# Kernel optimization log

Hardware: AMD Instinct MI355X
Metric: run time of the kernel (lower is better)

The kernel has to match this reference:

```python
import jax, jax.numpy as jnp
import numpy as np

N_NODES = 50000
N_EDGES = 800000
IN_C, HID, OUT_C = 128, 128, 16
N_GRAPHS = 128


def setup_inputs() -> dict:
    key = jax.random.key(0)
    ks = jax.random.split(key, 8)
    x = jax.random.normal(ks[0], (N_NODES, IN_C), dtype=jnp.float32)
    edge_index = jax.random.randint(ks[1], (2, N_EDGES), 0, N_NODES, dtype=jnp.int64)
    batch = jnp.sort(jax.random.randint(ks[2], (N_NODES,), 0, N_GRAPHS, dtype=jnp.int64))
    s1 = 1.0 / np.sqrt(IN_C)
    s2 = 1.0 / np.sqrt(HID)
    W1 = jax.random.normal(ks[3], (IN_C, HID), dtype=jnp.float32) * s1
    b1 = jnp.zeros((HID,), dtype=jnp.float32)
    W2 = jax.random.normal(ks[4], (HID, HID), dtype=jnp.float32) * s2
    b2 = jnp.zeros((HID,), dtype=jnp.float32)
    Wfc = jax.random.normal(ks[5], (HID, OUT_C), dtype=jnp.float32) * s2
    bfc = jnp.zeros((OUT_C,), dtype=jnp.float32)
    return {"x": x, "edge_index": edge_index, "batch": batch,
            "W1": W1, "b1": b1, "W2": W2, "b2": b2, "Wfc": Wfc, "bfc": bfc}


def _gcn_conv(x, W, b, src, dst, deg_inv_sqrt, n_nodes):
    # linear transform first (PyG order), then normalized sparse aggregation
    h = x @ W  # [N, H]
    norm = deg_inv_sqrt[src] * deg_inv_sqrt[dst]  # [E+N] (self-loops appended)
    msgs = h[src] * norm[:, None]  # [E+N, H] dominant gather
    agg = jax.ops.segment_sum(msgs, dst, num_segments=n_nodes)
    return agg + b


def reference(x, edge_index, batch, W1, b1, W2, b2, Wfc, bfc):
    n = x.shape[0]
    loops = jnp.arange(n, dtype=edge_index.dtype)
    src = jnp.concatenate([edge_index[0], loops])
    dst = jnp.concatenate([edge_index[1], loops])
    # symmetric normalization with self-loops: deg computed on dst
    deg = jax.ops.segment_sum(jnp.ones_like(src, dtype=x.dtype), dst, num_segments=n)
    deg_inv_sqrt = jnp.where(deg > 0, jax.lax.rsqrt(jnp.maximum(deg, 1.0)), 0.0)

    h = jax.nn.relu(_gcn_conv(x, W1, b1, src, dst, deg_inv_sqrt, n))
    h = jax.nn.relu(_gcn_conv(h, W2, b2, src, dst, deg_inv_sqrt, n))

    # global mean pool over graph ids
    sums = jax.ops.segment_sum(h, batch, num_segments=N_GRAPHS)
    counts = jax.ops.segment_sum(jnp.ones((n,), dtype=h.dtype), batch, num_segments=N_GRAPHS)
    pooled = sums / jnp.maximum(counts, 1.0)[:, None]  # [G, H]

    logits = pooled @ Wfc + bfc  # [G, OUT_C]
    return jax.nn.log_softmax(logits, axis=1)
```

## Files before the change

### kernel.cpp

```cpp
#include <hip/hip_runtime.h>

#define N_NODES  50000
#define N_EDGES  800000
#define HID      128
#define OUT_C    16
#define N_GRAPHS 128
#define MAXDEG   64
#define NSLICE   6250
#define EPB      8192
#define FILLB    784
#define GEMMB    782
#define PAD      136

typedef __attribute__((ext_vector_type(8))) short bf16x8;
typedef __attribute__((ext_vector_type(4))) float f32x4;
typedef __attribute__((ext_vector_type(8))) unsigned short us8;
typedef __attribute__((ext_vector_type(4))) unsigned short us4;

__device__ __forceinline__ unsigned short f2bf(float f) {
  unsigned u = __float_as_uint(f);
  u += 0x7fffu + ((u >> 16) & 1u);
  return (unsigned short)(u >> 16);
}

__device__ __forceinline__ void gemm_compute_store(
    unsigned short* sA, const float* __restrict__ W,
    unsigned short* __restrict__ T, int base) {
  const int tid = threadIdx.x;
  const int lane = tid & 63;
  const int w = tid >> 6;
  const int l15 = lane & 15;
  const int quad = lane >> 4;
  __syncthreads();

  f32x4 acc[4][2];
#pragma unroll
  for (int nt = 0; nt < 4; ++nt)
#pragma unroll
    for (int c = 0; c < 2; ++c) acc[nt][c] = (f32x4)(0.f);

  const int ct0 = w * 2;
  const int ncol = ct0 * 16 + l15;
#pragma unroll
  for (int ks = 0; ks < 4; ++ks) {
    const int koff = ks * 32 + quad * 8;
    bf16x8 a[4], bfr[2];
#pragma unroll
    for (int c = 0; c < 2; ++c) {
      const float* wp = W + (size_t)koff * HID + ncol + c * 16;
#pragma unroll
      for (int j = 0; j < 8; ++j) bfr[c][j] = (short)f2bf(wp[(size_t)j * HID]);
    }
#pragma unroll
    for (int nt = 0; nt < 4; ++nt)
      a[nt] = *(const bf16x8*)(sA + (nt * 16 + l15) * PAD + koff);
#pragma unroll
    for (int nt = 0; nt < 4; ++nt)
#pragma unroll
      for (int c = 0; c < 2; ++c)
        acc[nt][c] = __builtin_amdgcn_mfma_f32_16x16x32_bf16(a[nt], bfr[c], acc[nt][c], 0, 0, 0);
  }
  __syncthreads();

#pragma unroll
  for (int nt = 0; nt < 4; ++nt)
#pragma unroll
    for (int c = 0; c < 2; ++c)
#pragma unroll
      for (int r = 0; r < 4; ++r)
        sA[(nt * 16 + quad * 4 + r) * PAD + (ct0 + c) * 16 + l15] = f2bf(acc[nt][c][r]);
  __syncthreads();
#pragma unroll
  for (int i = 0; i < 4; ++i) {
    int idx = tid + i * 256;
    int nrow = idx >> 4;
    int col = (idx & 15) * 8;
    int node = base + nrow;
    if (node < N_NODES)
      *(us8*)(T + (size_t)node * HID + col) = *(const us8*)(sA + nrow * PAD + col);
  }
}

__device__ __forceinline__ void stage_a_f32(unsigned short* sA,
                                            const float* __restrict__ H, int base) {
#pragma unroll
  for (int i = 0; i < 8; ++i) {
    int idx = threadIdx.x + i * 256;
    int nrow = idx >> 5;
    int c4 = (idx & 31) * 4;
    float4 v = make_float4(0.f, 0.f, 0.f, 0.f);
    int node = base + nrow;
    if (node < N_NODES) v = *(const float4*)(H + (size_t)node * HID + c4);
    us4 b;
    b.x = f2bf(v.x); b.y = f2bf(v.y); b.z = f2bf(v.z); b.w = f2bf(v.w);
    *(us4*)(sA + nrow * PAD + c4) = b;
  }
}

__global__ __launch_bounds__(256) void mega_kernel(
    const int* __restrict__ src, const int* __restrict__ dst,
    int* __restrict__ deg, unsigned short* __restrict__ ell,
    const int* __restrict__ batch, int* __restrict__ start,
    const float* __restrict__ x, const float* __restrict__ W1,
    unsigned short* __restrict__ T) {
  __shared__ unsigned short sA[64 * PAD];
  int b = blockIdx.x;
  if (b < FILLB) {
    const int slice = b & 7;
    const int e0 = (b >> 3) * EPB;
    const int e1 = min(e0 + EPB, N_EDGES);
    const unsigned lo = slice * NSLICE;
    for (int e = e0 + threadIdx.x; e < e1; e += 256) {
      int d = __builtin_nontemporal_load(dst + e);
      if ((unsigned)(d - lo) < (unsigned)NSLICE) {
        int p = atomicAdd(&deg[d], 1);
        if (p < MAXDEG) ell[(d << 6) + p] = (unsigned short)src[e];
      }
    }
  } else if (b == FILLB) {
    int t = threadIdx.x;
    if (t <= N_GRAPHS) {
      int lo = 0, hi = N_NODES;
      while (lo < hi) {
        int mid = (lo + hi) >> 1;
        if (batch[mid] < t) lo = mid + 1; else hi = mid;
      }
      start[t] = lo;
    }
  } else {
    const int base = (b - FILLB - 1) * 64;
    stage_a_f32(sA, x, base);
    gemm_compute_store(sA, W1, T, base);
  }
}

__device__ __forceinline__ void agg_node(
    int node, int lane, const unsigned int* __restrict__ Tb,
    const unsigned short* __restrict__ ell, const int* __restrict__ deg,
    float bx, float by, float& ox, float& oy) {
  int dn = deg[node];
  float dd = rsqrtf((float)dn + 1.0f);
  unsigned sv = Tb[(size_t)node * 64 + lane];
  float wself = dd * dd;
  float ax = __int_as_float(sv << 16) * wself;
  float ay = __int_as_float(sv & 0xffff0000u) * wself;
  int m = min(dn, MAXDEG);
  int s0 = node << 6;
  int sidx = 0; float wv = 0.f;
  if (lane < m) {
    sidx = (int)ell[s0 + lane];
    wv = rsqrtf((float)deg[sidx] + 1.0f) * dd;
  }
  int j = 0;
  for (; j + 8 <= m; j += 8) {
#pragma unroll
    for (int q = 0; q < 8; ++q) {
      int s = __builtin_amdgcn_readlane(sidx, j + q);
      float w = __int_as_float(__builtin_amdgcn_readlane(__float_as_int(wv), j + q));
      unsigned t = Tb[(size_t)s * 64 + lane];
      ax += w * __int_as_float(t << 16);
      ay += w * __int_as_float(t & 0xffff0000u);
    }
  }
  for (; j < m; ++j) {
    int s = __builtin_amdgcn_readlane(sidx, j);
    float w = __int_as_float(__builtin_amdgcn_readlane(__float_as_int(wv), j));
    unsigned t = Tb[(size_t)s * 64 + lane];
    ax += w * __int_as_float(t << 16);
    ay += w * __int_as_float(t & 0xffff0000u);
  }
  ox = fmaxf(ax + bx, 0.f);
  oy = fmaxf(ay + by, 0.f);
}

__global__ __launch_bounds__(1024) void agg_gemm_kernel(
    const unsigned int* __restrict__ Tb, const unsigned short* __restrict__ ell,
    const int* __restrict__ deg, const float* __restrict__ bias,
    const float* __restrict__ W, unsigned short* __restrict__ T2) {
  __shared__ unsigned short sA[64 * PAD];
  const int tid = threadIdx.x;
  const int lane = tid & 63;
  const int w = tid >> 6;
  const int l15 = lane & 15;
  const int quad = lane >> 4;
  const int base = blockIdx.x * 64;

  float2 b = ((const float2*)bias)[lane];
#pragma unroll
  for (int i = 0; i < 4; ++i) {
    int nrow = w * 4 + i;
    int node = base + nrow;
    unsigned packed = 0;
    if (node < N_NODES) {
      float ox, oy;
      agg_node(node, lane, Tb, ell, deg, b.x, b.y, ox, oy);
      packed = (unsigned)f2bf(ox) | ((unsigned)f2bf(oy) << 16);
    }
    *(unsigned*)(sA + nrow * PAD + lane * 2) = packed;
  }
  __syncthreads();

  const int nt = w >> 2;
  const int ct0 = (w & 3) * 2;
  const int ncol = ct0 * 16 + l15;
  f32x4 acc[2];
  acc[0] = (f32x4)(0.f); acc[1] = (f32x4)(0.f);
#pragma unroll
  for (int ks = 0; ks < 4; ++ks) {
    const int koff = ks * 32 + quad * 8;
    bf16x8 a, bfr[2];
#pragma unroll
    for (int c = 0; c < 2; ++c) {
      const float* wp = W + (size_t)koff * HID + ncol + c * 16;
#pragma unroll
      for (int j = 0; j < 8; ++j) bfr[c][j] = (short)f2bf(wp[(size_t)j * HID]);
    }
    a = *(const bf16x8*)(sA + (nt * 16 + l15) * PAD + koff);
#pragma unroll
    for (int c = 0; c < 2; ++c)
      acc[c] = __builtin_amdgcn_mfma_f32_16x16x32_bf16(a, bfr[c], acc[c], 0, 0, 0);
  }
  __syncthreads();
#pragma unroll
  for (int c = 0; c < 2; ++c)
#pragma unroll
    for (int r = 0; r < 4; ++r)
      sA[(nt * 16 + quad * 4 + r) * PAD + (ct0 + c) * 16 + l15] = f2bf(acc[c][r]);
  __syncthreads();
  {
    int nrow = tid >> 4;
    int col = (tid & 15) * 8;
    int node = base + nrow;
    if (node < N_NODES)
      *(us8*)(T2 + (size_t)node * HID + col) = *(const us8*)(sA + nrow * PAD + col);
  }
}

__global__ __launch_bounds__(256) void aggregate_kernel(
    const unsigned int* __restrict__ Tb, const unsigned short* __restrict__ ell,
    const int* __restrict__ deg, const float* __restrict__ bias,
    unsigned int* __restrict__ Hb) {
  int node = (blockIdx.x * blockDim.x + threadIdx.x) >> 6;
  int lane = threadIdx.x & 63;
  if (node >= N_NODES) return;
  float2 b = ((const float2*)bias)[lane];
  float ox, oy;
  agg_node(node, lane, Tb, ell, deg, b.x, b.y, ox, oy);
  Hb[(size_t)node * 64 + lane] =
      (unsigned)f2bf(ox) | ((unsigned)f2bf(oy) << 16);
}

__global__ __launch_bounds__(256) void pool_head_kernel(
    const unsigned int* __restrict__ Hb, const int* __restrict__ start,
    const float* __restrict__ Wfc, const float* __restrict__ bfc,
    float* __restrict__ out) {
  __shared__ float2 red[4][64];
  __shared__ float spool[HID];
  int g = blockIdx.x;
  int n0 = start[g], n1 = start[g + 1];
  int lane = threadIdx.x & 63, w = threadIdx.x >> 6;
  float ax = 0.f, ay = 0.f;
  for (int n = n0 + w; n < n1; n += 4) {
    unsigned h = Hb[(size_t)n * 64 + lane];
    ax += __int_as_float(h << 16);
    ay += __int_as_float(h & 0xffff0000u);
  }
  red[w][lane] = make_float2(ax, ay);
  __syncthreads();
  if (threadIdx.x < 64) {
    float2 a = red[0][lane], b1 = red[1][lane], c = red[2][lane], d = red[3][lane];
    float inv = 1.0f / fmaxf((float)(n1 - n0), 1.0f);
    spool[lane * 2]     = (a.x + b1.x + c.x + d.x) * inv;
    spool[lane * 2 + 1] = (a.y + b1.y + c.y + d.y) * inv;
  }
  __syncthreads();
  if (threadIdx.x < 64) {
    int o = lane & 15;
    float part = 0.f;
    for (int k = (lane >> 4); k < HID; k += 4)
      part += spool[k] * Wfc[k * OUT_C + o];
    part += __shfl_xor(part, 16);
    part += __shfl_xor(part, 32);
    float logit = part + bfc[o];
    float m = logit;
#pragma unroll
    for (int d = 8; d >= 1; d >>= 1) m = fmaxf(m, __shfl_xor(m, d, 16));
    float e = __expf(logit - m);
    float s = e;
#pragma unroll
    for (int d = 8; d >= 1; d >>= 1) s += __shfl_xor(s, d, 16);
    float r = logit - m - __logf(s);
    if (lane < 16) out[g * OUT_C + o] = r;
  }
}

extern "C" void kernel_launch(void* const* d_in, const int* in_sizes, int n_in,
                              void* d_out, int out_size, void* d_ws, size_t ws_size,
                              hipStream_t stream) {
  const float* x    = (const float*)d_in[0];
  const int*   ei   = (const int*)d_in[1];
  const int*   batch= (const int*)d_in[2];
  const float* W1   = (const float*)d_in[3];
  const float* b1   = (const float*)d_in[4];
  const float* W2   = (const float*)d_in[5];
  const float* b2   = (const float*)d_in[6];
  const float* Wfc  = (const float*)d_in[7];
  const float* bfc  = (const float*)d_in[8];
  float* out = (float*)d_out;
  const int* src = ei;
  const int* dst = ei + N_EDGES;

  char* p = (char*)d_ws;
  auto alloc = [&](size_t bytes) { char* r = p; p += (bytes + 255) & ~255ull; return r; };
  int*   degI   = (int*)alloc((size_t)N_NODES * 4);
  int*   start  = (int*)alloc((N_GRAPHS + 1) * 4);
  unsigned short* ell = (unsigned short*)alloc((size_t)N_NODES * MAXDEG * 2);
  unsigned short* T   = (unsigned short*)alloc((size_t)N_NODES * HID * 2);
  unsigned short* T2  = (unsigned short*)alloc((size_t)N_NODES * HID * 2);
  unsigned short* Hb  = (unsigned short*)alloc((size_t)N_NODES * HID * 2);

  hipMemsetAsync(degI, 0, (size_t)N_NODES * 4, stream);

  int agg_blocks = (N_NODES * 64 + 255) / 256;

  mega_kernel<<<FILLB + 1 + GEMMB, 256, 0, stream>>>(src, dst, degI, ell,
                                                     batch, start, x, W1, T);
  agg_gemm_kernel<<<GEMMB, 1024, 0, stream>>>((const unsigned int*)T, ell, degI,
                                              b1, W2, T2);
  aggregate_kernel<<<agg_blocks, 256, 0, stream>>>((const unsigned int*)T2, ell, degI, b2,
                                                   (unsigned int*)Hb);
  pool_head_kernel<<<N_GRAPHS, 256, 0, stream>>>((const unsigned int*)Hb, start,
                                                 Wfc, bfc, out);
}
```

Before: 261.4 us.

## Shrink agg_gemm tiles to 16 nodes and split pooling across blocks with atomics

Result: faster. 245.0 us (-6.3%).

```diff
diff --git a/kernel.cpp b/kernel.cpp
--- a/kernel.cpp
+++ b/kernel.cpp
@@ -10,6 +10,7 @@
 #define EPB      8192
 #define FILLB    784
 #define GEMMB    782
+#define AGB      3125
 #define PAD      136
 
 typedef __attribute__((ext_vector_type(8))) short bf16x8;
@@ -177,62 +178,48 @@
     const unsigned int* __restrict__ Tb, const unsigned short* __restrict__ ell,
     const int* __restrict__ deg, const float* __restrict__ bias,
     const float* __restrict__ W, unsigned short* __restrict__ T2) {
-  __shared__ unsigned short sA[64 * PAD];
+  __shared__ unsigned short sA[16 * PAD];
   const int tid = threadIdx.x;
   const int lane = tid & 63;
   const int w = tid >> 6;
   const int l15 = lane & 15;
   const int quad = lane >> 4;
-  const int base = blockIdx.x * 64;
-
-  float2 b = ((const float2*)bias)[lane];
-#pragma unroll
-  for (int i = 0; i < 4; ++i) {
-    int nrow = w * 4 + i;
-    int node = base + nrow;
-    unsigned packed = 0;
-    if (node < N_NODES) {
-      float ox, oy;
-      agg_node(node, lane, Tb, ell, deg, b.x, b.y, ox, oy);
-      packed = (unsigned)f2bf(ox) | ((unsigned)f2bf(oy) << 16);
-    }
-    *(unsigned*)(sA + nrow * PAD + lane * 2) = packed;
-  }
-  __syncthreads();
-
-  const int nt = w >> 2;
-  const int ct0 = (w & 3) * 2;
-  const int ncol = ct0 * 16 + l15;
-  f32x4 acc[2];
-  acc[0] = (f32x4)(0.f); acc[1] = (f32x4)(0.f);
-#pragma unroll
-  for (int ks = 0; ks < 4; ++ks) {
-    const int koff = ks * 32 + quad * 8;
-    bf16x8 a, bfr[2];
-#pragma unroll
-    for (int c = 0; c < 2; ++c) {
-      const float* wp = W + (size_t)koff * HID + ncol + c * 16;
-#pragma unroll
-      for (int j = 0; j < 8; ++j) bfr[c][j] = (short)f2bf(wp[(size_t)j * HID]);
-    }
-    a = *(const bf16x8*)(sA + (nt * 16 + l15) * PAD + koff);
-#pragma unroll
-    for (int c = 0; c < 2; ++c)
-      acc[c] = __builtin_amdgcn_mfma_f32_16x16x32_bf16(a, bfr[c], acc[c], 0, 0, 0);
-  }
-  __syncthreads();
-#pragma unroll
-  for (int c = 0; c < 2; ++c)
+  const int base = blockIdx.x * 16;
+
+  {
+    float2 b = ((const float2*)bias)[lane];
+    float ox, oy;
+    agg_node(base + w, lane, Tb, ell, deg, b.x, b.y, ox, oy);
+    *(unsigned*)(sA + w * PAD + lane * 2) =
+        (unsigned)f2bf(ox) | ((unsigned)f2bf(oy) << 16);
+  }
+  __syncthreads();
+
+  f32x4 acc = (f32x4)(0.f);
+  if (w < 8) {
+    const int ncol = w * 16 + l15;
+#pragma unroll
+    for (int ks = 0; ks < 4; ++ks) {
+      const int koff = ks * 32 + quad * 8;
+      bf16x8 a = *(const bf16x8*)(sA + l15 * PAD + koff);
+      bf16x8 bfr;
+      const float* wp = W + (size_t)koff * HID + ncol;
+#pragma unroll
+      for (int j = 0; j < 8; ++j) bfr[j] = (short)f2bf(wp[(size_t)j * HID]);
+      acc = __builtin_amdgcn_mfma_f32_16x16x32_bf16(a, bfr, acc, 0, 0, 0);
+    }
+  }
+  __syncthreads();
+  if (w < 8) {
 #pragma unroll
     for (int r = 0; r < 4; ++r)
-      sA[(nt * 16 + quad * 4 + r) * PAD + (ct0 + c) * 16 + l15] = f2bf(acc[c][r]);
-  __syncthreads();
-  {
+      sA[(quad * 4 + r) * PAD + w * 16 + l15] = f2bf(acc[r]);
+  }
+  __syncthreads();
+  if (tid < 256) {
     int nrow = tid >> 4;
     int col = (tid & 15) * 8;
-    int node = base + nrow;
-    if (node < N_NODES)
-      *(us8*)(T2 + (size_t)node * HID + col) = *(const us8*)(sA + nrow * PAD + col);
+    *(us8*)(T2 + (size_t)(base + nrow) * HID + col) = *(const us8*)(sA + nrow * PAD + col);
   }
 }
 
@@ -250,17 +237,16 @@
       (unsigned)f2bf(ox) | ((unsigned)f2bf(oy) << 16);
 }
 
-__global__ __launch_bounds__(256) void pool_head_kernel(
+__global__ __launch_bounds__(256) void pool_partial_kernel(
     const unsigned int* __restrict__ Hb, const int* __restrict__ start,
-    const float* __restrict__ Wfc, const float* __restrict__ bfc,
-    float* __restrict__ out) {
+    float* __restrict__ pooled) {
   __shared__ float2 red[4][64];
-  __shared__ float spool[HID];
-  int g = blockIdx.x;
+  int g = blockIdx.x >> 2;
+  int chunk = blockIdx.x & 3;
   int n0 = start[g], n1 = start[g + 1];
   int lane = threadIdx.x & 63, w = threadIdx.x >> 6;
   float ax = 0.f, ay = 0.f;
-  for (int n = n0 + w; n < n1; n += 4) {
+  for (int n = n0 + chunk * 4 + w; n < n1; n += 16) {
     unsigned h = Hb[(size_t)n * 64 + lane];
     ax += __int_as_float(h << 16);
     ay += __int_as_float(h & 0xffff0000u);
@@ -268,30 +254,35 @@
   red[w][lane] = make_float2(ax, ay);
   __syncthreads();
   if (threadIdx.x < 64) {
-    float2 a = red[0][lane], b1 = red[1][lane], c = red[2][lane], d = red[3][lane];
-    float inv = 1.0f / fmaxf((float)(n1 - n0), 1.0f);
-    spool[lane * 2]     = (a.x + b1.x + c.x + d.x) * inv;
-    spool[lane * 2 + 1] = (a.y + b1.y + c.y + d.y) * inv;
-  }
-  __syncthreads();
-  if (threadIdx.x < 64) {
-    int o = lane & 15;
-    float part = 0.f;
-    for (int k = (lane >> 4); k < HID; k += 4)
-      part += spool[k] * Wfc[k * OUT_C + o];
-    part += __shfl_xor(part, 16);
-    part += __shfl_xor(part, 32);
-    float logit = part + bfc[o];
-    float m = logit;
-#pragma unroll
-    for (int d = 8; d >= 1; d >>= 1) m = fmaxf(m, __shfl_xor(m, d, 16));
-    float e = __expf(logit - m);
-    float s = e;
-#pragma unroll
-    for (int d = 8; d >= 1; d >>= 1) s += __shfl_xor(s, d, 16);
-    float r = logit - m - __logf(s);
-    if (lane < 16) out[g * OUT_C + o] = r;
-  }
+    float2 a = red[0][lane], b = red[1][lane], c = red[2][lane], d = red[3][lane];
+    atomicAdd(&pooled[g * HID + lane * 2],     a.x + b.x + c.x + d.x);
+    atomicAdd(&pooled[g * HID + lane * 2 + 1], a.y + b.y + c.y + d.y);
+  }
+}
+
+__global__ __launch_bounds__(64) void head_kernel(
+    const float* __restrict__ pooled, const int* __restrict__ start,
+    const float* __restrict__ Wfc, const float* __restrict__ bfc,
+    float* __restrict__ out) {
+  int g = blockIdx.x;
+  int lane = threadIdx.x;
+  int o = lane & 15;
+  float inv = 1.0f / fmaxf((float)(start[g + 1] - start[g]), 1.0f);
+  float part = 0.f;
+  for (int k = (lane >> 4); k < HID; k += 4)
+    part += pooled[g * HID + k] * inv * Wfc[k * OUT_C + o];
+  part += __shfl_xor(part, 16);
+  part += __shfl_xor(part, 32);
+  float logit = part + bfc[o];
+  float m = logit;
+#pragma unroll
+  for (int d = 8; d >= 1; d >>= 1) m = fmaxf(m, __shfl_xor(m, d, 16));
+  float e = __expf(logit - m);
+  float s = e;
+#pragma unroll
+  for (int d = 8; d >= 1; d >>= 1) s += __shfl_xor(s, d, 16);
+  float r = logit - m - __logf(s);
+  if (lane < 16) out[g * OUT_C + o] = r;
 }
 
 extern "C" void kernel_launch(void* const* d_in, const int* in_sizes, int n_in,
@@ -314,21 +305,24 @@
   auto alloc = [&](size_t bytes) { char* r = p; p += (bytes + 255) & ~255ull; return r; };
   int*   degI   = (int*)alloc((size_t)N_NODES * 4);
   int*   start  = (int*)alloc((N_GRAPHS + 1) * 4);
+  float* pooled = (float*)alloc((size_t)N_GRAPHS * HID * 4);
   unsigned short* ell = (unsigned short*)alloc((size_t)N_NODES * MAXDEG * 2);
   unsigned short* T   = (unsigned short*)alloc((size_t)N_NODES * HID * 2);
   unsigned short* T2  = (unsigned short*)alloc((size_t)N_NODES * HID * 2);
   unsigned short* Hb  = (unsigned short*)alloc((size_t)N_NODES * HID * 2);
 
   hipMemsetAsync(degI, 0, (size_t)N_NODES * 4, stream);
+  hipMemsetAsync(pooled, 0, (size_t)N_GRAPHS * HID * 4, stream);
 
   int agg_blocks = (N_NODES * 64 + 255) / 256;
 
   mega_kernel<<<FILLB + 1 + GEMMB, 256, 0, stream>>>(src, dst, degI, ell,
                                                      batch, start, x, W1, T);
-  agg_gemm_kernel<<<GEMMB, 1024, 0, stream>>>((const unsigned int*)T, ell, degI,
-                                              b1, W2, T2);
+  agg_gemm_kernel<<<AGB, 1024, 0, stream>>>((const unsigned int*)T, ell, degI,
+                                            b1, W2, T2);
   aggregate_kernel<<<agg_blocks, 256, 0, stream>>>((const unsigned int*)T2, ell, degI, b2,
                                                    (unsigned int*)Hb);
-  pool_head_kernel<<<N_GRAPHS, 256, 0, stream>>>((const unsigned int*)Hb, start,
-                                                 Wfc, bfc, out);
-}
+  pool_partial_kernel<<<N_GRAPHS * 4, 256, 0, stream>>>((const unsigned int*)Hb, start,
+                                                        pooled);
+  head_kernel<<<N_GRAPHS, 64, 0, stream>>>(pooled, start, Wfc, bfc, out);
+}
```
